# Optimization experiments

Measured on AMD Instinct MI355X. Metric: run time of the kernel, lower is better.

Reference implementation:

```python
import jax, jax.numpy as jnp
import numpy as np

N = 50000      # nodes
E = 800000     # edges (avg degree 16)
F_IN = 128     # num_features
H1 = 256       # hidden_dims[0]
H2 = 128       # hidden_dims[1]
D_EMB = 64     # embedding_dim
C_CLS = 2      # num_classes
EPS = 1e-5     # BatchNorm eps


def setup_inputs() -> dict:
    key = jax.random.key(0)
    ks = jax.random.split(key, 24)
    f32 = jnp.float32
    def w(k, shape, scale=0.05):
        return jax.random.normal(k, shape, f32) * scale
    inp = {
        "x": jax.random.normal(ks[0], (N, F_IN), f32),
        "edge_index": jax.random.randint(ks[1], (2, E), 0, N, jnp.int32),
        # input_proj
        "Wp": w(ks[2], (F_IN, H1)), "bp": jnp.zeros((H1,), f32),
        # conv1 (SAGEConv): lin_l (neighbors, with bias), lin_r (root, no bias)
        "W1l": w(ks[3], (F_IN, H1)), "b1l": jnp.zeros((H1,), f32), "W1r": w(ks[4], (F_IN, H1)),
        # bn1 (eval mode, running stats)
        "bn1_g": jnp.ones((H1,), f32), "bn1_b": jnp.zeros((H1,), f32),
        "bn1_m": w(ks[5], (H1,), 0.01), "bn1_v": jnp.ones((H1,), f32) + 0.1 * jax.random.uniform(ks[6], (H1,), f32),
        # skip_proj
        "Wsk": w(ks[7], (H1, H2)), "bsk": jnp.zeros((H2,), f32),
        # conv2
        "W2l": w(ks[8], (H1, H2)), "b2l": jnp.zeros((H2,), f32), "W2r": w(ks[9], (H1, H2)),
        # bn2
        "bn2_g": jnp.ones((H2,), f32), "bn2_b": jnp.zeros((H2,), f32),
        "bn2_m": w(ks[10], (H2,), 0.01), "bn2_v": jnp.ones((H2,), f32) + 0.1 * jax.random.uniform(ks[11], (H2,), f32),
        # conv3
        "W3l": w(ks[12], (H2, D_EMB)), "b3l": jnp.zeros((D_EMB,), f32), "W3r": w(ks[13], (H2, D_EMB)),
        # classifier
        "Wc": w(ks[14], (D_EMB, C_CLS)), "bc": jnp.zeros((C_CLS,), f32),
    }
    return inp


def _sage(h, src, dst, Wl, bl, Wr):
    # mean aggregation of source features into destination nodes
    s = jax.ops.segment_sum(h[src], dst, num_segments=N)        # [N, d]
    cnt = jax.ops.segment_sum(jnp.ones((src.shape[0], 1), h.dtype), dst, num_segments=N)
    mean = s / jnp.maximum(cnt, 1.0)
    return mean @ Wl + bl + h @ Wr


def _bn(h, g, b, m, v):
    return (h - m) * jax.lax.rsqrt(v + EPS) * g + b


def reference(x, edge_index, Wp, bp, W1l, b1l, W1r, bn1_g, bn1_b, bn1_m, bn1_v,
              Wsk, bsk, W2l, b2l, W2r, bn2_g, bn2_b, bn2_m, bn2_v,
              W3l, b3l, W3r, Wc, bc):
    src, dst = edge_index[0], edge_index[1]
    identity = x @ Wp + bp                                # input_proj
    h = _sage(x, src, dst, W1l, b1l, W1r)                 # conv1
    h = jax.nn.relu(_bn(h, bn1_g, bn1_b, bn1_m, bn1_v) + identity)
    # dropout is identity in eval mode
    identity = h @ Wsk + bsk                              # skip_proj
    h = _sage(h, src, dst, W2l, b2l, W2r)                 # conv2
    h = jax.nn.relu(_bn(h, bn2_g, bn2_b, bn2_m, bn2_v) + identity)
    emb = _sage(h, src, dst, W3l, b3l, W3r)               # conv3
    logits = emb @ Wc + bc
    return (logits, emb)
```

## Files before the change

kernel.cpp:

```cpp
#include <hip/hip_runtime.h>
#include <hip/hip_fp16.h>

#define NN 50000
#define NE 800000
#define SLN 6250
#define CAP 64
#define BCAP 106496
constexpr float EPSV = 1e-5f;

typedef __attribute__((ext_vector_type(8))) short short8;
typedef __attribute__((ext_vector_type(4))) float f32x4;

__device__ __forceinline__ float bf2f(unsigned short u) {
    return __uint_as_float(((unsigned int)u) << 16);
}
__device__ __forceinline__ unsigned short f2bf(float f) {
    unsigned int x = __float_as_uint(f);
    return (unsigned short)((x + 0x7FFFu + ((x >> 16) & 1u)) >> 16);
}
__device__ __forceinline__ unsigned char f2e5(float f) {
    unsigned short h = __half_as_ushort(__float2half(f));
    unsigned short r = h + 0x7F + ((h >> 8) & 1);
    return (unsigned char)(r >> 8);
}
__device__ __forceinline__ void acc16(float* a, uint4 u) {
#pragma unroll
    for (int q = 0; q < 4; q++) {
        unsigned int x = (q == 0) ? u.x : (q == 1) ? u.y : (q == 2) ? u.z : u.w;
        unsigned int h01 = ((x << 8) & 0xFF00u) | ((x << 16) & 0xFF000000u);
        unsigned int h23 = ((x >> 8) & 0xFF00u) | (x & 0xFF000000u);
        __half2 p01 = *(__half2*)&h01, p23 = *(__half2*)&h23;
        float2 f01 = __half22float2(p01), f23 = __half22float2(p23);
        a[q * 4 + 0] += f01.x; a[q * 4 + 1] += f01.y;
        a[q * 4 + 2] += f23.x; a[q * 4 + 3] += f23.y;
    }
}

__global__ __launch_bounds__(256) void k_bin(const int* __restrict__ src,
                                             const int* __restrict__ dst,
                                             int* __restrict__ binCnt,
                                             int2* __restrict__ binBuf) {
    __shared__ int hcnt[8];
    __shared__ int hbase[8];
    int tid = threadIdx.x;
    if (tid < 8) hcnt[tid] = 0;
    __syncthreads();
    int q = blockIdx.x * 256 + tid;
    bool val = q < NE / 4;
    int4 d = make_int4(0, 0, 0, 0), s = make_int4(0, 0, 0, 0);
    int b0 = 0, b1 = 0, b2 = 0, b3 = 0, r0 = 0, r1 = 0, r2 = 0, r3 = 0;
    if (val) {
        d = ((const int4*)dst)[q];
        s = ((const int4*)src)[q];
        b0 = d.x / SLN; r0 = atomicAdd(&hcnt[b0], 1);
        b1 = d.y / SLN; r1 = atomicAdd(&hcnt[b1], 1);
        b2 = d.z / SLN; r2 = atomicAdd(&hcnt[b2], 1);
        b3 = d.w / SLN; r3 = atomicAdd(&hcnt[b3], 1);
    }
    __syncthreads();
    if (tid < 8) hbase[tid] = atomicAdd(&binCnt[tid], hcnt[tid]);
    __syncthreads();
    if (val) {
        binBuf[(size_t)b0 * BCAP + hbase[b0] + r0] = make_int2(d.x, s.x);
        binBuf[(size_t)b1 * BCAP + hbase[b1] + r1] = make_int2(d.y, s.y);
        binBuf[(size_t)b2 * BCAP + hbase[b2] + r2] = make_int2(d.z, s.z);
        binBuf[(size_t)b3 * BCAP + hbase[b3] + r3] = make_int2(d.w, s.w);
    }
}

__global__ __launch_bounds__(256) void k_scatter2(const int2* __restrict__ binBuf,
                                                  const int* __restrict__ binCnt,
                                                  int* __restrict__ cnt,
                                                  int* __restrict__ csr) {
    int bin = blockIdx.x & 7;
    int lb = blockIdx.x >> 3;
    int n = binCnt[bin];
    const int2* buf = binBuf + (size_t)bin * BCAP;
    for (int i = lb * 256 + threadIdx.x; i < n; i += 128 * 256) {
        int2 p = buf[i];
        int slot = atomicAdd(&cnt[p.x], 1);
        csr[p.x * CAP + slot] = p.y;
    }
}

__device__ void prep1_body(int t, const float* Wp, const float* bp, const float* W1l,
                           const float* b1l, const float* W1r, const float* g, const float* b,
                           const float* m, const float* v, unsigned short* Wf, float* c) {
    int lane = t & 63, f = (t >> 6) & 3, kt = (t >> 8) & 7;
    int nb = t >> 11;
    int col = nb * 64 + f * 16 + (lane & 15);
    int k0 = kt * 32 + (lane >> 4) * 8;
    float A = g[col] * rsqrtf(v[col] + EPSV);
    unsigned short* o = Wf + (size_t)t * 8;
    for (int j = 0; j < 8; j++) {
        int k = k0 + j;
        float w;
        if (k < 128) w = W1l[k * 256 + col] * A;
        else         w = W1r[(k - 128) * 256 + col] * A + Wp[(k - 128) * 256 + col];
        o[j] = f2bf(w);
    }
    if (t < 256) {
        float At = g[t] * rsqrtf(v[t] + EPSV);
        c[t] = b1l[t] * At + (b[t] - m[t] * At) + bp[t];
    }
}

__device__ void prep2_body(int t, const float* Wsk, const float* bsk, const float* W2l,
                           const float* b2l, const float* W2r, const float* g, const float* b,
                           const float* m, const float* v, unsigned short* Wf, float* c) {
    int lane = t & 63, f = (t >> 6) & 3, kt = (t >> 8) & 7, nb = t >> 11;
    int col = nb * 64 + f * 16 + (lane & 15);
    int k0 = kt * 32 + (lane >> 4) * 8;
    unsigned short* o = Wf + (size_t)t * 8;
    if (col < 128) {
        float A = g[col] * rsqrtf(v[col] + EPSV);
        for (int j = 0; j < 8; j++) o[j] = f2bf(W2l[(k0 + j) * 128 + col] * A);
    } else {
        int cc = col - 128;
        float A = g[cc] * rsqrtf(v[cc] + EPSV);
        for (int j = 0; j < 8; j++)
            o[j] = f2bf(W2r[(k0 + j) * 128 + cc] * A + Wsk[(k0 + j) * 128 + cc]);
    }
    if (t < 128) {
        float At = g[t] * rsqrtf(v[t] + EPSV);
        c[t] = b2l[t] * At + (b[t] - m[t] * At) + bsk[t];
    }
}

__device__ void prep3_body(int t, const float* W3l, const float* b3l, const float* W3r,
                           unsigned short* Wf, float* c) {
    int lane = t & 63, f = (t >> 6) & 3, kt = (t >> 8) & 3, nb = t >> 10;
    int col = nb * 64 + f * 16 + (lane & 15);
    int k0 = kt * 32 + (lane >> 4) * 8;
    unsigned short* o = Wf + (size_t)t * 8;
    if (col < 64) {
        for (int j = 0; j < 8; j++) o[j] = f2bf(W3l[(k0 + j) * 64 + col]);
    } else {
        int cc = col - 64;
        for (int j = 0; j < 8; j++) o[j] = f2bf(W3r[(k0 + j) * 64 + cc]);
    }
    if (t < 64) c[t] = b3l[t];
}

__global__ void k_prep_fused(const float* x, unsigned short* xcat, unsigned char* xf8,
                             int* cnt, int* binCnt,
                             const float* Wp, const float* bp,
                             const float* W1l, const float* b1l, const float* W1r,
                             const float* g1, const float* b1, const float* m1, const float* v1,
                             const float* Wsk, const float* bsk,
                             const float* W2l, const float* b2l, const float* W2r,
                             const float* g2, const float* b2, const float* m2, const float* v2,
                             const float* W3l, const float* b3l, const float* W3r,
                             unsigned short* Wf1, unsigned short* Wf2, unsigned short* Wf3,
                             float* c1, float* c2, float* c3) {
    int bb = blockIdx.x;
    if (bb < 6250) {
        int i = bb * 256 + threadIdx.x;
        if (i < NN / 4) ((int4*)cnt)[i] = make_int4(0, 0, 0, 0);
        if (i < 2) ((int4*)binCnt)[i] = make_int4(0, 0, 0, 0);
        if (i >= NN * 128 / 4) return;
        int r = i >> 5, c4 = (i & 31) * 4;
        float4 v = ((const float4*)x)[i];
        ushort4 u = make_ushort4(f2bf(v.x), f2bf(v.y), f2bf(v.z), f2bf(v.w));
        *(ushort4*)&xcat[(size_t)r * 256 + 128 + c4] = u;
        uchar4 u8 = make_uchar4(f2e5(v.x), f2e5(v.y), f2e5(v.z), f2e5(v.w));
        *(uchar4*)&xf8[(size_t)r * 128 + c4] = u8;
    } else if (bb < 6282) {
        prep1_body((bb - 6250) * 256 + threadIdx.x, Wp, bp, W1l, b1l, W1r, g1, b1, m1, v1, Wf1, c1);
    } else if (bb < 6314) {
        prep2_body((bb - 6282) * 256 + threadIdx.x, Wsk, bsk, W2l, b2l, W2r, g2, b2, m2, v2, Wf2, c2);
    } else {
        prep3_body((bb - 6314) * 256 + threadIdx.x, W3l, b3l, W3r, Wf3, c3);
    }
}

template <int K, int TOTN, int MODE>
__global__ __launch_bounds__(256) void k_gemm(const unsigned short* __restrict__ A,
                                              const unsigned short* __restrict__ Wf,
                                              const float* __restrict__ bias,
                                              unsigned short* __restrict__ Out,
                                              unsigned char* __restrict__ Pf8) {
    constexpr int KT = K / 32;
    constexpr int NB = TOTN / 64;
    __shared__ unsigned short Bs[K * 64];
    int tid = threadIdx.x;
    int lane = tid & 63, w = tid >> 6;
    int bm = blockIdx.x;

    int r0 = bm * 128 + w * 32;
    int ra0 = r0 + (lane & 15);
    int ra1 = ra0 + 16;
    if (ra0 >= NN) ra0 = NN - 1;
    if (ra1 >= NN) ra1 = NN - 1;
    const unsigned short* ap0 = A + (size_t)ra0 * K + ((lane >> 4) * 8);
    const unsigned short* ap1 = A + (size_t)ra1 * K + ((lane >> 4) * 8);
    short8 afr0[KT], afr1[KT];
#pragma unroll
    for (int kt = 0; kt < KT; kt++) {
        afr0[kt] = *(const short8*)(ap0 + kt * 32);
        afr1[kt] = *(const short8*)(ap1 + kt * 32);
    }

    int rb = r0 + (lane >> 4) * 4;

    for (int nb = 0; nb < NB; nb++) {
        __syncthreads();
        {
            const float4* srcp = (const float4*)(Wf + (size_t)nb * K * 64);
            float4* dsts = (float4*)Bs;
            for (int i = tid; i < K * 8; i += 256) dsts[i] = srcp[i];
        }
        __syncthreads();

        f32x4 acc[2][4];
#pragma unroll
        for (int i = 0; i < 2; i++)
#pragma unroll
            for (int f = 0; f < 4; f++) acc[i][f] = (f32x4){0.f, 0.f, 0.f, 0.f};
#pragma unroll
        for (int kt = 0; kt < KT; kt++) {
#pragma unroll
            for (int f = 0; f < 4; f++) {
                short8 bfr = *(const short8*)&Bs[((kt * 4 + f) * 64 + lane) * 8];
                acc[0][f] = __builtin_amdgcn_mfma_f32_16x16x32_bf16(afr0[kt], bfr, acc[0][f], 0, 0, 0);
                acc[1][f] = __builtin_amdgcn_mfma_f32_16x16x32_bf16(afr1[kt], bfr, acc[1][f], 0, 0, 0);
            }
        }

        int cc = nb * 64 + (lane & 15);
#pragma unroll
        for (int af = 0; af < 2; af++) {
#pragma unroll
            for (int f = 0; f < 4; f++) {
                float bv = (MODE == 1) ? bias[cc + f * 16] : 0.f;
#pragma unroll
                for (int r = 0; r < 4; r++) {
                    int gr = rb + af * 16 + r;
                    if (gr < NN) {
                        float val = acc[af][f][r];
                        if (MODE == 1) val = fmaxf(val + bv, 0.f);
                        int col = cc + f * 16;
                        if (MODE == 2) {
                            if (col < 128) Pf8[(size_t)gr * 128 + col] = f2e5(val);
                            else           Out[(size_t)gr * 128 + (col - 128)] = f2bf(val);
                        } else {
                            Out[(size_t)gr * TOTN + col] = f2bf(val);
                        }
                    }
                }
            }
        }
    }
}


__global__ __launch_bounds__(256) void k_aggx(const int* __restrict__ cnt,
                                              const int* __restrict__ csr,
                                              const unsigned char* __restrict__ xf8,
                                              unsigned short* __restrict__ xcat) {
    int lane = threadIdx.x & 63, wv = threadIdx.x >> 6;
    int node = blockIdx.x * 4 + wv;
    int deg = cnt[node];
    const int* cp = csr + node * CAP;
    int g = lane >> 3, l8 = lane & 7;
    float a[16];
#pragma unroll
    for (int j = 0; j < 16; j++) a[j] = 0.f;
    const unsigned char* base = xf8 + l8 * 16;
    int e = 0;
    for (; e + 16 <= deg; e += 16) {
        int s0 = cp[e + g], s1 = cp[e + 8 + g];
        uint4 u0 = *(const uint4*)(base + (size_t)s0 * 128);
        uint4 u1 = *(const uint4*)(base + (size_t)s1 * 128);
        acc16(a, u0); acc16(a, u1);
    }
    if (e + g < deg) {
        uint4 u = *(const uint4*)(base + (size_t)cp[e + g] * 128);
        acc16(a, u);
    }
    if (e + 8 + g < deg) {
        uint4 u = *(const uint4*)(base + (size_t)cp[e + 8 + g] * 128);
        acc16(a, u);
    }
#pragma unroll
    for (int j = 0; j < 16; j++) {
        a[j] += __shfl_xor(a[j], 8);
        a[j] += __shfl_xor(a[j], 16);
        a[j] += __shfl_xor(a[j], 32);
    }
    if (lane < 8) {
        float inv = 1.f / (float)max(deg, 1);
        unsigned short o[16];
#pragma unroll
        for (int j = 0; j < 16; j++) o[j] = f2bf(a[j] * inv);
        *(short8*)&xcat[(size_t)node * 256 + lane * 16] = *(short8*)&o[0];
        *(short8*)&xcat[(size_t)node * 256 + lane * 16 + 8] = *(short8*)&o[8];
    }
}

__global__ __launch_bounds__(256) void k_agg2(const unsigned char* __restrict__ pf8,
                                              const unsigned short* __restrict__ r2,
                                              const int* __restrict__ cnt,
                                              const int* __restrict__ csr,
                                              const float* __restrict__ c,
                                              unsigned short* __restrict__ h2) {
    int lane = threadIdx.x & 63, wv = threadIdx.x >> 6;
    int node = blockIdx.x * 4 + wv;
    int deg = cnt[node];
    const int* cp = csr + node * CAP;
    int g = lane >> 3, l8 = lane & 7;
    float a[16];
#pragma unroll
    for (int j = 0; j < 16; j++) a[j] = 0.f;
    const unsigned char* base = pf8 + l8 * 16;
    int e = 0;
    for (; e + 16 <= deg; e += 16) {
        int s0 = cp[e + g], s1 = cp[e + 8 + g];
        uint4 u0 = *(const uint4*)(base + (size_t)s0 * 128);
        uint4 u1 = *(const uint4*)(base + (size_t)s1 * 128);
        acc16(a, u0); acc16(a, u1);
    }
    if (e + g < deg) {
        uint4 u = *(const uint4*)(base + (size_t)cp[e + g] * 128);
        acc16(a, u);
    }
    if (e + 8 + g < deg) {
        uint4 u = *(const uint4*)(base + (size_t)cp[e + 8 + g] * 128);
        acc16(a, u);
    }
#pragma unroll
    for (int j = 0; j < 16; j++) {
        a[j] += __shfl_xor(a[j], 8);
        a[j] += __shfl_xor(a[j], 16);
        a[j] += __shfl_xor(a[j], 32);
    }
    if (lane < 8) {
        float inv = 1.f / (float)max(deg, 1);
        short8 rA = *(const short8*)&r2[(size_t)node * 128 + lane * 16];
        short8 rB = *(const short8*)&r2[(size_t)node * 128 + lane * 16 + 8];
        const float* cpb = c + lane * 16;
        unsigned short o[16];
#pragma unroll
        for (int j = 0; j < 8; j++)
            o[j] = f2bf(fmaxf(a[j] * inv + bf2f(rA[j]) + cpb[j], 0.f));
#pragma unroll
        for (int j = 0; j < 8; j++)
            o[8 + j] = f2bf(fmaxf(a[8 + j] * inv + bf2f(rB[j]) + cpb[8 + j], 0.f));
        *(short8*)&h2[(size_t)node * 128 + lane * 16] = *(short8*)&o[0];
        *(short8*)&h2[(size_t)node * 128 + lane * 16 + 8] = *(short8*)&o[8];
    }
}

__global__ __launch_bounds__(256) void k_agg_final(const unsigned short* __restrict__ G,
                                                   const int* __restrict__ cnt,
                                                   const int* __restrict__ csr,
                                                   const float* __restrict__ c,
                                                   const float* __restrict__ Wc,
                                                   const float* __restrict__ bc,
                                                   float* __restrict__ outbuf) {
    int lane = threadIdx.x & 63, wv = threadIdx.x >> 6;
    int node = blockIdx.x * 4 + wv;
    int deg = cnt[node];
    const int* cp = csr + node * CAP;
    int g = lane >> 3, l8 = lane & 7;
    float a[8];
#pragma unroll
    for (int j = 0; j < 8; j++) a[j] = 0.f;
    const unsigned short* base = G + l8 * 8;
    int e = 0;
    for (; e + 32 <= deg; e += 32) {
        int s0 = cp[e + g], s1 = cp[e + 8 + g], s2 = cp[e + 16 + g], s3 = cp[e + 24 + g];
        short8 u0 = *(const short8*)(base + (size_t)s0 * 128);
        short8 u1 = *(const short8*)(base + (size_t)s1 * 128);
        short8 u2 = *(const short8*)(base + (size_t)s2 * 128);
        short8 u3 = *(const short8*)(base + (size_t)s3 * 128);
#pragma unroll
        for (int j = 0; j < 8; j++)
            a[j] += (bf2f(u0[j]) + bf2f(u1[j])) + (bf2f(u2[j]) + bf2f(u3[j]));
    }
    for (; e + 8 <= deg; e += 8) {
        short8 u = *(const short8*)(base + (size_t)cp[e + g] * 128);
#pragma unroll
        for (int j = 0; j < 8; j++) a[j] += bf2f(u[j]);
    }
    if (e + g < deg) {
        short8 u = *(const short8*)(base + (size_t)cp[e + g] * 128);
#pragma unroll
        for (int j = 0; j < 8; j++) a[j] += bf2f(u[j]);
    }
#pragma unroll
    for (int j = 0; j < 8; j++) {
        a[j] += __shfl_xor(a[j], 8);
        a[j] += __shfl_xor(a[j], 16);
        a[j] += __shfl_xor(a[j], 32);
    }
    float l0 = 0.f, l1 = 0.f;
    if (lane < 8) {
        float inv = 1.f / (float)max(deg, 1);
        short8 r = *(const short8*)&G[(size_t)node * 128 + 64 + l8 * 8];
        const float* cpb = c + l8 * 8;
        float v[8];
#pragma unroll
        for (int j = 0; j < 8; j++) v[j] = a[j] * inv + bf2f(r[j]) + cpb[j];
        float* emb = outbuf + 2 * (size_t)NN;
        *(float4*)&emb[(size_t)node * 64 + l8 * 8] = make_float4(v[0], v[1], v[2], v[3]);
        *(float4*)&emb[(size_t)node * 64 + l8 * 8 + 4] = make_float4(v[4], v[5], v[6], v[7]);
        int c0 = l8 * 8;
#pragma unroll
        for (int j = 0; j < 8; j++) {
            l0 += v[j] * Wc[2 * (c0 + j)];
            l1 += v[j] * Wc[2 * (c0 + j) + 1];
        }
    }
    l0 += __shfl_xor(l0, 1); l1 += __shfl_xor(l1, 1);
    l0 += __shfl_xor(l0, 2); l1 += __shfl_xor(l1, 2);
    l0 += __shfl_xor(l0, 4); l1 += __shfl_xor(l1, 4);
    if (lane == 0) {
        outbuf[(size_t)node * 2 + 0] = l0 + bc[0];
        outbuf[(size_t)node * 2 + 1] = l1 + bc[1];
    }
}

extern "C" void kernel_launch(void* const* d_in, const int* in_sizes, int n_in,
                              void* d_out, int out_size, void* d_ws, size_t ws_size,
                              hipStream_t stream) {
    const float* x    = (const float*)d_in[0];
    const int*   ei   = (const int*)d_in[1];
    const float* Wp   = (const float*)d_in[2];
    const float* bp   = (const float*)d_in[3];
    const float* W1l  = (const float*)d_in[4];
    const float* b1l  = (const float*)d_in[5];
    const float* W1r  = (const float*)d_in[6];
    const float* bn1g = (const float*)d_in[7];
    const float* bn1b = (const float*)d_in[8];
    const float* bn1m = (const float*)d_in[9];
    const float* bn1v = (const float*)d_in[10];
    const float* Wsk  = (const float*)d_in[11];
    const float* bsk  = (const float*)d_in[12];
    const float* W2l  = (const float*)d_in[13];
    const float* b2l  = (const float*)d_in[14];
    const float* W2r  = (const float*)d_in[15];
    const float* bn2g = (const float*)d_in[16];
    const float* bn2b = (const float*)d_in[17];
    const float* bn2m = (const float*)d_in[18];
    const float* bn2v = (const float*)d_in[19];
    const float* W3l  = (const float*)d_in[20];
    const float* b3l  = (const float*)d_in[21];
    const float* W3r  = (const float*)d_in[22];
    const float* Wc   = (const float*)d_in[23];
    const float* bc   = (const float*)d_in[24];

    const int* src = ei;
    const int* dst = ei + NE;

    char* ws = (char*)d_ws;
    size_t o = 0;
    auto alloc = [&](size_t b) -> char* {
        char* p = ws + o;
        o = (o + b + 255) & ~(size_t)255;
        return p;
    };
    int* cnt    = (int*)alloc((size_t)NN * 4);
    int* binCnt = (int*)alloc(64);
    int* csr    = (int*)alloc((size_t)NN * CAP * 4);
    unsigned char*  xf8  = (unsigned char*)alloc((size_t)NN * 128);
    unsigned short* xcat = (unsigned short*)alloc((size_t)NN * 256 * 2);
    unsigned short* h1   = (unsigned short*)alloc((size_t)NN * 256 * 2);
    unsigned char*  pf8  = (unsigned char*)alloc((size_t)NN * 128);
    unsigned short* r2   = (unsigned short*)alloc((size_t)NN * 128 * 2);
    unsigned short* h2   = (unsigned short*)alloc((size_t)NN * 128 * 2);
    unsigned short* G3   = (unsigned short*)alloc((size_t)NN * 128 * 2);
    unsigned short* Wf1  = (unsigned short*)alloc((size_t)256 * 256 * 2);
    unsigned short* Wf2  = (unsigned short*)alloc((size_t)256 * 256 * 2);
    unsigned short* Wf3  = (unsigned short*)alloc((size_t)128 * 128 * 2);
    float* c1 = (float*)alloc(256 * 4);
    float* c2 = (float*)alloc(128 * 4);
    float* c3 = (float*)alloc(64 * 4);
    int2* binBuf = (int2*)G3;

    float* outbuf = (float*)d_out;

    k_prep_fused<<<6322, 256, 0, stream>>>(x, xcat, xf8, cnt, binCnt,
                                           Wp, bp, W1l, b1l, W1r, bn1g, bn1b, bn1m, bn1v,
                                           Wsk, bsk, W2l, b2l, W2r, bn2g, bn2b, bn2m, bn2v,
                                           W3l, b3l, W3r, Wf1, Wf2, Wf3, c1, c2, c3);

    k_bin<<<782, 256, 0, stream>>>(src, dst, binCnt, binBuf);
    k_scatter2<<<1024, 256, 0, stream>>>(binBuf, binCnt, cnt, csr);

    k_aggx<<<12500, 256, 0, stream>>>(cnt, csr, xf8, xcat);
    k_gemm<256, 256, 1><<<391, 256, 0, stream>>>(xcat, Wf1, c1, h1, nullptr);

    k_gemm<256, 256, 2><<<391, 256, 0, stream>>>(h1, Wf2, nullptr, r2, pf8);
    k_agg2<<<12500, 256, 0, stream>>>(pf8, r2, cnt, csr, c2, h2);

    k_gemm<128, 128, 0><<<391, 256, 0, stream>>>(h2, Wf3, nullptr, G3, nullptr);
    k_agg_final<<<12500, 256, 0, stream>>>(G3, cnt, csr, c3, Wc, bc, outbuf);
}
```

Measured before the change: 210.8 us.

## Fuse edge binning into prep kernel, split GEMM N across grid, narrow aggregation

Edge binning moves from its own kernel into extra blocks of the fused prep kernel, and binCnt is now zeroed with a memset, which removes one launch. The GEMMs now launch one block per 64-column tile through blockIdx.y instead of looping over tiles inside a block, which gives more parallel blocks but reloads the A fragments once per tile. The fp8 aggregation kernels use 16 lanes of 8 bytes per row instead of 8 lanes of 16 bytes, so each pass covers 4 edges. The conv3 output is split into separate contiguous P3 and R3 arrays so the final gather reads 128-byte rows.

```diff
diff --git a/kernel.cpp b/kernel.cpp
--- a/kernel.cpp
+++ b/kernel.cpp
@@ -23,63 +23,16 @@
     unsigned short r = h + 0x7F + ((h >> 8) & 1);
     return (unsigned char)(r >> 8);
 }
-__device__ __forceinline__ void acc16(float* a, uint4 u) {
-#pragma unroll
-    for (int q = 0; q < 4; q++) {
-        unsigned int x = (q == 0) ? u.x : (q == 1) ? u.y : (q == 2) ? u.z : u.w;
+__device__ __forceinline__ void acc8(float* a, uint2 u) {
+#pragma unroll
+    for (int q = 0; q < 2; q++) {
+        unsigned int x = (q == 0) ? u.x : u.y;
         unsigned int h01 = ((x << 8) & 0xFF00u) | ((x << 16) & 0xFF000000u);
         unsigned int h23 = ((x >> 8) & 0xFF00u) | (x & 0xFF000000u);
-        __half2 p01 = *(__half2*)&h01, p23 = *(__half2*)&h23;
-        float2 f01 = __half22float2(p01), f23 = __half22float2(p23);
+        float2 f01 = __half22float2(*(__half2*)&h01);
+        float2 f23 = __half22float2(*(__half2*)&h23);
         a[q * 4 + 0] += f01.x; a[q * 4 + 1] += f01.y;
         a[q * 4 + 2] += f23.x; a[q * 4 + 3] += f23.y;
-    }
-}
-
-__global__ __launch_bounds__(256) void k_bin(const int* __restrict__ src,
-                                             const int* __restrict__ dst,
-                                             int* __restrict__ binCnt,
-                                             int2* __restrict__ binBuf) {
-    __shared__ int hcnt[8];
-    __shared__ int hbase[8];
-    int tid = threadIdx.x;
-    if (tid < 8) hcnt[tid] = 0;
-    __syncthreads();
-    int q = blockIdx.x * 256 + tid;
-    bool val = q < NE / 4;
-    int4 d = make_int4(0, 0, 0, 0), s = make_int4(0, 0, 0, 0);
-    int b0 = 0, b1 = 0, b2 = 0, b3 = 0, r0 = 0, r1 = 0, r2 = 0, r3 = 0;
-    if (val) {
-        d = ((const int4*)dst)[q];
-        s = ((const int4*)src)[q];
-        b0 = d.x / SLN; r0 = atomicAdd(&hcnt[b0], 1);
-        b1 = d.y / SLN; r1 = atomicAdd(&hcnt[b1], 1);
-        b2 = d.z / SLN; r2 = atomicAdd(&hcnt[b2], 1);
-        b3 = d.w / SLN; r3 = atomicAdd(&hcnt[b3], 1);
-    }
-    __syncthreads();
-    if (tid < 8) hbase[tid] = atomicAdd(&binCnt[tid], hcnt[tid]);
-    __syncthreads();
-    if (val) {
-        binBuf[(size_t)b0 * BCAP + hbase[b0] + r0] = make_int2(d.x, s.x);
-        binBuf[(size_t)b1 * BCAP + hbase[b1] + r1] = make_int2(d.y, s.y);
-        binBuf[(size_t)b2 * BCAP + hbase[b2] + r2] = make_int2(d.z, s.z);
-        binBuf[(size_t)b3 * BCAP + hbase[b3] + r3] = make_int2(d.w, s.w);
-    }
-}
-
-__global__ __launch_bounds__(256) void k_scatter2(const int2* __restrict__ binBuf,
-                                                  const int* __restrict__ binCnt,
-                                                  int* __restrict__ cnt,
-                                                  int* __restrict__ csr) {
-    int bin = blockIdx.x & 7;
-    int lb = blockIdx.x >> 3;
-    int n = binCnt[bin];
-    const int2* buf = binBuf + (size_t)bin * BCAP;
-    for (int i = lb * 256 + threadIdx.x; i < n; i += 128 * 256) {
-        int2 p = buf[i];
-        int slot = atomicAdd(&cnt[p.x], 1);
-        csr[p.x * CAP + slot] = p.y;
     }
 }
 
@@ -144,6 +97,7 @@
 
 __global__ void k_prep_fused(const float* x, unsigned short* xcat, unsigned char* xf8,
                              int* cnt, int* binCnt,
+                             const int* src, const int* dst, int2* binBuf,
                              const float* Wp, const float* bp,
                              const float* W1l, const float* b1l, const float* W1r,
                              const float* g1, const float* b1, const float* m1, const float* v1,
@@ -153,11 +107,13 @@
                              const float* W3l, const float* b3l, const float* W3r,
                              unsigned short* Wf1, unsigned short* Wf2, unsigned short* Wf3,
                              float* c1, float* c2, float* c3) {
+    __shared__ int hcnt[8];
+    __shared__ int hbase[8];
     int bb = blockIdx.x;
+    int tid = threadIdx.x;
     if (bb < 6250) {
-        int i = bb * 256 + threadIdx.x;
+        int i = bb * 256 + tid;
         if (i < NN / 4) ((int4*)cnt)[i] = make_int4(0, 0, 0, 0);
-        if (i < 2) ((int4*)binCnt)[i] = make_int4(0, 0, 0, 0);
         if (i >= NN * 128 / 4) return;
         int r = i >> 5, c4 = (i & 31) * 4;
         float4 v = ((const float4*)x)[i];
@@ -166,11 +122,50 @@
         uchar4 u8 = make_uchar4(f2e5(v.x), f2e5(v.y), f2e5(v.z), f2e5(v.w));
         *(uchar4*)&xf8[(size_t)r * 128 + c4] = u8;
     } else if (bb < 6282) {
-        prep1_body((bb - 6250) * 256 + threadIdx.x, Wp, bp, W1l, b1l, W1r, g1, b1, m1, v1, Wf1, c1);
+        prep1_body((bb - 6250) * 256 + tid, Wp, bp, W1l, b1l, W1r, g1, b1, m1, v1, Wf1, c1);
     } else if (bb < 6314) {
-        prep2_body((bb - 6282) * 256 + threadIdx.x, Wsk, bsk, W2l, b2l, W2r, g2, b2, m2, v2, Wf2, c2);
+        prep2_body((bb - 6282) * 256 + tid, Wsk, bsk, W2l, b2l, W2r, g2, b2, m2, v2, Wf2, c2);
+    } else if (bb < 6322) {
+        prep3_body((bb - 6314) * 256 + tid, W3l, b3l, W3r, Wf3, c3);
     } else {
-        prep3_body((bb - 6314) * 256 + threadIdx.x, W3l, b3l, W3r, Wf3, c3);
+        if (tid < 8) hcnt[tid] = 0;
+        __syncthreads();
+        int q = (bb - 6322) * 256 + tid;
+        bool val = q < NE / 4;
+        int4 d = make_int4(0, 0, 0, 0), s = make_int4(0, 0, 0, 0);
+        int b0 = 0, b1i = 0, b2i = 0, b3i = 0, r0 = 0, r1 = 0, r2 = 0, r3 = 0;
+        if (val) {
+            d = ((const int4*)dst)[q];
+            s = ((const int4*)src)[q];
+            b0 = d.x / SLN; r0 = atomicAdd(&hcnt[b0], 1);
+            b1i = d.y / SLN; r1 = atomicAdd(&hcnt[b1i], 1);
+            b2i = d.z / SLN; r2 = atomicAdd(&hcnt[b2i], 1);
+            b3i = d.w / SLN; r3 = atomicAdd(&hcnt[b3i], 1);
+        }
+        __syncthreads();
+        if (tid < 8) hbase[tid] = atomicAdd(&binCnt[tid], hcnt[tid]);
+        __syncthreads();
+        if (val) {
+            binBuf[(size_t)b0 * BCAP + hbase[b0] + r0] = make_int2(d.x, s.x);
+            binBuf[(size_t)b1i * BCAP + hbase[b1i] + r1] = make_int2(d.y, s.y);
+            binBuf[(size_t)b2i * BCAP + hbase[b2i] + r2] = make_int2(d.z, s.z);
+            binBuf[(size_t)b3i * BCAP + hbase[b3i] + r3] = make_int2(d.w, s.w);
+        }
+    }
+}
+
+__global__ __launch_bounds__(256) void k_scatter2(const int2* __restrict__ binBuf,
+                                                  const int* __restrict__ binCnt,
+                                                  int* __restrict__ cnt,
+                                                  int* __restrict__ csr) {
+    int bin = blockIdx.x & 7;
+    int lb = blockIdx.x >> 3;
+    int n = binCnt[bin];
+    const int2* buf = binBuf + (size_t)bin * BCAP;
+    for (int i = lb * 256 + threadIdx.x; i < n; i += 128 * 256) {
+        int2 p = buf[i];
+        int slot = atomicAdd(&cnt[p.x], 1);
+        csr[p.x * CAP + slot] = p.y;
     }
 }
 
@@ -179,13 +174,13 @@
                                               const unsigned short* __restrict__ Wf,
                                               const float* __restrict__ bias,
                                               unsigned short* __restrict__ Out,
+                                              unsigned short* __restrict__ Out2,
                                               unsigned char* __restrict__ Pf8) {
     constexpr int KT = K / 32;
-    constexpr int NB = TOTN / 64;
     __shared__ unsigned short Bs[K * 64];
     int tid = threadIdx.x;
     int lane = tid & 63, w = tid >> 6;
-    int bm = blockIdx.x;
+    int bm = blockIdx.x, nb = blockIdx.y;
 
     int r0 = bm * 128 + w * 32;
     int ra0 = r0 + (lane & 15);
@@ -201,51 +196,50 @@
         afr1[kt] = *(const short8*)(ap1 + kt * 32);
     }
 
+    {
+        const float4* srcp = (const float4*)(Wf + (size_t)nb * K * 64);
+        float4* dsts = (float4*)Bs;
+        for (int i = tid; i < K * 8; i += 256) dsts[i] = srcp[i];
+    }
+    __syncthreads();
+
+    f32x4 acc[2][4];
+#pragma unroll
+    for (int i = 0; i < 2; i++)
+#pragma unroll
+        for (int f = 0; f < 4; f++) acc[i][f] = (f32x4){0.f, 0.f, 0.f, 0.f};
+#pragma unroll
+    for (int kt = 0; kt < KT; kt++) {
+#pragma unroll
+        for (int f = 0; f < 4; f++) {
+            short8 bfr = *(const short8*)&Bs[((kt * 4 + f) * 64 + lane) * 8];
+            acc[0][f] = __builtin_amdgcn_mfma_f32_16x16x32_bf16(afr0[kt], bfr, acc[0][f], 0, 0, 0);
+            acc[1][f] = __builtin_amdgcn_mfma_f32_16x16x32_bf16(afr1[kt], bfr, acc[1][f], 0, 0, 0);
+        }
+    }
+
+    int cc = nb * 64 + (lane & 15);
     int rb = r0 + (lane >> 4) * 4;
-
-    for (int nb = 0; nb < NB; nb++) {
-        __syncthreads();
-        {
-            const float4* srcp = (const float4*)(Wf + (size_t)nb * K * 64);
-            float4* dsts = (float4*)Bs;
-            for (int i = tid; i < K * 8; i += 256) dsts[i] = srcp[i];
-        }
-        __syncthreads();
-
-        f32x4 acc[2][4];
-#pragma unroll
-        for (int i = 0; i < 2; i++)
-#pragma unroll
-            for (int f = 0; f < 4; f++) acc[i][f] = (f32x4){0.f, 0.f, 0.f, 0.f};
-#pragma unroll
-        for (int kt = 0; kt < KT; kt++) {
-#pragma unroll
-            for (int f = 0; f < 4; f++) {
-                short8 bfr = *(const short8*)&Bs[((kt * 4 + f) * 64 + lane) * 8];
-                acc[0][f] = __builtin_amdgcn_mfma_f32_16x16x32_bf16(afr0[kt], bfr, acc[0][f], 0, 0, 0);
-                acc[1][f] = __builtin_amdgcn_mfma_f32_16x16x32_bf16(afr1[kt], bfr, acc[1][f], 0, 0, 0);
-            }
-        }
-
-        int cc = nb * 64 + (lane & 15);
-#pragma unroll
-        for (int af = 0; af < 2; af++) {
-#pragma unroll
-            for (int f = 0; f < 4; f++) {
-                float bv = (MODE == 1) ? bias[cc + f * 16] : 0.f;
-#pragma unroll
-                for (int r = 0; r < 4; r++) {
-                    int gr = rb + af * 16 + r;
-                    if (gr < NN) {
-                        float val = acc[af][f][r];
-                        if (MODE == 1) val = fmaxf(val + bv, 0.f);
-                        int col = cc + f * 16;
-                        if (MODE == 2) {
-                            if (col < 128) Pf8[(size_t)gr * 128 + col] = f2e5(val);
-                            else           Out[(size_t)gr * 128 + (col - 128)] = f2bf(val);
-                        } else {
-                            Out[(size_t)gr * TOTN + col] = f2bf(val);
-                        }
+#pragma unroll
+    for (int af = 0; af < 2; af++) {
+#pragma unroll
+        for (int f = 0; f < 4; f++) {
+            int col = cc + f * 16;
+            float bv = (MODE == 1) ? bias[col] : 0.f;
+#pragma unroll
+            for (int r = 0; r < 4; r++) {
+                int gr = rb + af * 16 + r;
+                if (gr < NN) {
+                    float val = acc[af][f][r];
+                    if (MODE == 1) val = fmaxf(val + bv, 0.f);
+                    if (MODE == 2) {
+                        if (col < 128) Pf8[(size_t)gr * 128 + col] = f2e5(val);
+                        else           Out[(size_t)gr * 128 + (col - 128)] = f2bf(val);
+                    } else if (MODE == 3) {
+                        if (col < 64) Out[(size_t)gr * 64 + col] = f2bf(val);
+                        else          Out2[(size_t)gr * 64 + (col - 64)] = f2bf(val);
+                    } else {
+                        Out[(size_t)gr * TOTN + col] = f2bf(val);
                     }
                 }
             }
@@ -262,39 +256,38 @@
     int node = blockIdx.x * 4 + wv;
     int deg = cnt[node];
     const int* cp = csr + node * CAP;
-    int g = lane >> 3, l8 = lane & 7;
-    float a[16];
-#pragma unroll
-    for (int j = 0; j < 16; j++) a[j] = 0.f;
-    const unsigned char* base = xf8 + l8 * 16;
+    int g = lane >> 4, l16 = lane & 15;
+    float a[8];
+#pragma unroll
+    for (int j = 0; j < 8; j++) a[j] = 0.f;
+    const unsigned char* base = xf8 + l16 * 8;
     int e = 0;
-    for (; e + 16 <= deg; e += 16) {
-        int s0 = cp[e + g], s1 = cp[e + 8 + g];
-        uint4 u0 = *(const uint4*)(base + (size_t)s0 * 128);
-        uint4 u1 = *(const uint4*)(base + (size_t)s1 * 128);
-        acc16(a, u0); acc16(a, u1);
+    for (; e + 8 <= deg; e += 8) {
+        int s0 = cp[e + g], s1 = cp[e + 4 + g];
+        uint2 u0 = *(const uint2*)(base + (size_t)s0 * 128);
+        uint2 u1 = *(const uint2*)(base + (size_t)s1 * 128);
+        acc8(a, u0); acc8(a, u1);
+    }
+    if (e + 4 <= deg) {
+        uint2 u = *(const uint2*)(base + (size_t)cp[e + g] * 128);
+        acc8(a, u);
+        e += 4;
     }
     if (e + g < deg) {
-        uint4 u = *(const uint4*)(base + (size_t)cp[e + g] * 128);
-        acc16(a, u);
-    }
-    if (e + 8 + g < deg) {
-        uint4 u = *(const uint4*)(base + (size_t)cp[e + 8 + g] * 128);
-        acc16(a, u);
-    }
-#pragma unroll
-    for (int j = 0; j < 16; j++) {
-        a[j] += __shfl_xor(a[j], 8);
+        uint2 u = *(const uint2*)(base + (size_t)cp[e + g] * 128);
+        acc8(a, u);
+    }
+#pragma unroll
+    for (int j = 0; j < 8; j++) {
         a[j] += __shfl_xor(a[j], 16);
         a[j] += __shfl_xor(a[j], 32);
     }
-    if (lane < 8) {
+    if (lane < 16) {
         float inv = 1.f / (float)max(deg, 1);
-        unsigned short o[16];
-#pragma unroll
-        for (int j = 0; j < 16; j++) o[j] = f2bf(a[j] * inv);
-        *(short8*)&xcat[(size_t)node * 256 + lane * 16] = *(short8*)&o[0];
-        *(short8*)&xcat[(size_t)node * 256 + lane * 16 + 8] = *(short8*)&o[8];
+        unsigned short o[8];
+#pragma unroll
+        for (int j = 0; j < 8; j++) o[j] = f2bf(a[j] * inv);
+        *(short8*)&xcat[(size_t)node * 256 + l16 * 8] = *(short8*)&o[0];
     }
 }
 
@@ -308,50 +301,46 @@
     int node = blockIdx.x * 4 + wv;
     int deg = cnt[node];
     const int* cp = csr + node * CAP;
-    int g = lane >> 3, l8 = lane & 7;
-    float a[16];
-#pragma unroll
-    for (int j = 0; j < 16; j++) a[j] = 0.f;
-    const unsigned char* base = pf8 + l8 * 16;
+    int g = lane >> 4, l16 = lane & 15;
+    float a[8];
+#pragma unroll
+    for (int j = 0; j < 8; j++) a[j] = 0.f;
+    const unsigned char* base = pf8 + l16 * 8;
     int e = 0;
-    for (; e + 16 <= deg; e += 16) {
-        int s0 = cp[e + g], s1 = cp[e + 8 + g];
-        uint4 u0 = *(const uint4*)(base + (size_t)s0 * 128);
-        uint4 u1 = *(const uint4*)(base + (size_t)s1 * 128);
-        acc16(a, u0); acc16(a, u1);
+    for (; e + 8 <= deg; e += 8) {
+        int s0 = cp[e + g], s1 = cp[e + 4 + g];
+        uint2 u0 = *(const uint2*)(base + (size_t)s0 * 128);
+        uint2 u1 = *(const uint2*)(base + (size_t)s1 * 128);
+        acc8(a, u0); acc8(a, u1);
+    }
+    if (e + 4 <= deg) {
+        uint2 u = *(const uint2*)(base + (size_t)cp[e + g] * 128);
+        acc8(a, u);
+        e += 4;
     }
     if (e + g < deg) {
-        uint4 u = *(const uint4*)(base + (size_t)cp[e + g] * 128);
-        acc16(a, u);
-    }
-    if (e + 8 + g < deg) {
-        uint4 u = *(const uint4*)(base + (size_t)cp[e + 8 + g] * 128);
-        acc16(a, u);
-    }
-#pragma unroll
-    for (int j = 0; j < 16; j++) {
-        a[j] += __shfl_xor(a[j], 8);
+        uint2 u = *(const uint2*)(base + (size_t)cp[e + g] * 128);
+        acc8(a, u);
+    }
+#pragma unroll
+    for (int j = 0; j < 8; j++) {
         a[j] += __shfl_xor(a[j], 16);
         a[j] += __shfl_xor(a[j], 32);
     }
-    if (lane < 8) {
+    if (lane < 16) {
         float inv = 1.f / (float)max(deg, 1);
-        short8 rA = *(const short8*)&r2[(size_t)node * 128 + lane * 16];
-        short8 rB = *(const short8*)&r2[(size_t)node * 128 + lane * 16 + 8];
-        const float* cpb = c + lane * 16;
-        unsigned short o[16];
+        short8 r = *(const short8*)&r2[(size_t)node * 128 + l16 * 8];
+        const float* cpb = c + l16 * 8;
+        unsigned short o[8];
 #pragma unroll
         for (int j = 0; j < 8; j++)
-            o[j] = f2bf(fmaxf(a[j] * inv + bf2f(rA[j]) + cpb[j], 0.f));
-#pragma unroll
-        for (int j = 0; j < 8; j++)
-            o[8 + j] = f2bf(fmaxf(a[8 + j] * inv + bf2f(rB[j]) + cpb[8 + j], 0.f));
-        *(short8*)&h2[(size_t)node * 128 + lane * 16] = *(short8*)&o[0];
-        *(short8*)&h2[(size_t)node * 128 + lane * 16 + 8] = *(short8*)&o[8];
-    }
-}
-
-__global__ __launch_bounds__(256) void k_agg_final(const unsigned short* __restrict__ G,
+            o[j] = f2bf(fmaxf(a[j] * inv + bf2f(r[j]) + cpb[j], 0.f));
+        *(short8*)&h2[(size_t)node * 128 + l16 * 8] = *(short8*)&o[0];
+    }
+}
+
+__global__ __launch_bounds__(256) void k_agg_final(const unsigned short* __restrict__ P3,
+                                                   const unsigned short* __restrict__ R3,
                                                    const int* __restrict__ cnt,
                                                    const int* __restrict__ csr,
                                                    const float* __restrict__ c,
@@ -366,25 +355,25 @@
     float a[8];
 #pragma unroll
     for (int j = 0; j < 8; j++) a[j] = 0.f;
-    const unsigned short* base = G + l8 * 8;
+    const unsigned short* base = P3 + l8 * 8;
     int e = 0;
     for (; e + 32 <= deg; e += 32) {
         int s0 = cp[e + g], s1 = cp[e + 8 + g], s2 = cp[e + 16 + g], s3 = cp[e + 24 + g];
-        short8 u0 = *(const short8*)(base + (size_t)s0 * 128);
-        short8 u1 = *(const short8*)(base + (size_t)s1 * 128);
-        short8 u2 = *(const short8*)(base + (size_t)s2 * 128);
-        short8 u3 = *(const short8*)(base + (size_t)s3 * 128);
+        short8 u0 = *(const short8*)(base + (size_t)s0 * 64);
+        short8 u1 = *(const short8*)(base + (size_t)s1 * 64);
+        short8 u2 = *(const short8*)(base + (size_t)s2 * 64);
+        short8 u3 = *(const short8*)(base + (size_t)s3 * 64);
 #pragma unroll
         for (int j = 0; j < 8; j++)
             a[j] += (bf2f(u0[j]) + bf2f(u1[j])) + (bf2f(u2[j]) + bf2f(u3[j]));
     }
     for (; e + 8 <= deg; e += 8) {
-        short8 u = *(const short8*)(base + (size_t)cp[e + g] * 128);
+        short8 u = *(const short8*)(base + (size_t)cp[e + g] * 64);
 #pragma unroll
         for (int j = 0; j < 8; j++) a[j] += bf2f(u[j]);
     }
     if (e + g < deg) {
-        short8 u = *(const short8*)(base + (size_t)cp[e + g] * 128);
+        short8 u = *(const short8*)(base + (size_t)cp[e + g] * 64);
 #pragma unroll
         for (int j = 0; j < 8; j++) a[j] += bf2f(u[j]);
     }
@@ -397,7 +386,7 @@
     float l0 = 0.f, l1 = 0.f;
     if (lane < 8) {
         float inv = 1.f / (float)max(deg, 1);
-        short8 r = *(const short8*)&G[(size_t)node * 128 + 64 + l8 * 8];
+        short8 r = *(const short8*)&R3[(size_t)node * 64 + l8 * 8];
         const float* cpb = c + l8 * 8;
         float v[8];
 #pragma unroll
@@ -469,31 +458,32 @@
     unsigned char*  pf8  = (unsigned char*)alloc((size_t)NN * 128);
     unsigned short* r2   = (unsigned short*)alloc((size_t)NN * 128 * 2);
     unsigned short* h2   = (unsigned short*)alloc((size_t)NN * 128 * 2);
-    unsigned short* G3   = (unsigned short*)alloc((size_t)NN * 128 * 2);
+    unsigned short* P3   = (unsigned short*)alloc((size_t)NN * 64 * 2);
+    unsigned short* R3   = (unsigned short*)alloc((size_t)NN * 64 * 2);
     unsigned short* Wf1  = (unsigned short*)alloc((size_t)256 * 256 * 2);
     unsigned short* Wf2  = (unsigned short*)alloc((size_t)256 * 256 * 2);
     unsigned short* Wf3  = (unsigned short*)alloc((size_t)128 * 128 * 2);
     float* c1 = (float*)alloc(256 * 4);
     float* c2 = (float*)alloc(128 * 4);
     float* c3 = (float*)alloc(64 * 4);
-    int2* binBuf = (int2*)G3;
+    int2* binBuf = (int2*)P3;
 
     float* outbuf = (float*)d_out;
 
-    k_prep_fused<<<6322, 256, 0, stream>>>(x, xcat, xf8, cnt, binCnt,
+    hipMemsetAsync(binCnt, 0, 64, stream);
+    k_prep_fused<<<7104, 256, 0, stream>>>(x, xcat, xf8, cnt, binCnt, src, dst, binBuf,
                                            Wp, bp, W1l, b1l, W1r, bn1g, bn1b, bn1m, bn1v,
                                            Wsk, bsk, W2l, b2l, W2r, bn2g, bn2b, bn2m, bn2v,
                                            W3l, b3l, W3r, Wf1, Wf2, Wf3, c1, c2, c3);
 
-    k_bin<<<782, 256, 0, stream>>>(src, dst, binCnt, binBuf);
     k_scatter2<<<1024, 256, 0, stream>>>(binBuf, binCnt, cnt, csr);
 
     k_aggx<<<12500, 256, 0, stream>>>(cnt, csr, xf8, xcat);
-    k_gemm<256, 256, 1><<<391, 256, 0, stream>>>(xcat, Wf1, c1, h1, nullptr);
-
-    k_gemm<256, 256, 2><<<391, 256, 0, stream>>>(h1, Wf2, nullptr, r2, pf8);
+    k_gemm<256, 256, 1><<<dim3(391, 4), 256, 0, stream>>>(xcat, Wf1, c1, h1, nullptr, nullptr);
+
+    k_gemm<256, 256, 2><<<dim3(391, 4), 256, 0, stream>>>(h1, Wf2, nullptr, r2, nullptr, pf8);
     k_agg2<<<12500, 256, 0, stream>>>(pf8, r2, cnt, csr, c2, h2);
 
-    k_gemm<128, 128, 0><<<391, 256, 0, stream>>>(h2, Wf3, nullptr, G3, nullptr);
-    k_agg_final<<<12500, 256, 0, stream>>>(G3, cnt, csr, c3, Wc, bc, outbuf);
-}
+    k_gemm<128, 128, 3><<<dim3(391, 2), 256, 0, stream>>>(h2, Wf3, nullptr, P3, R3, nullptr);
+    k_agg_final<<<12500, 256, 0, stream>>>(P3, R3, cnt, csr, c3, Wc, bc, outbuf);
+}
```

After: 217.6 us. 3.2% more time.
